# Performance work log

Hardware: AMD Instinct MI355X
Metric: run time of the kernel (lower is better)

## Reference

```python
import jax, jax.numpy as jnp
import numpy as np

B, S, D, H, F = 16, 512, 1024, 16, 4096
DH = D // H
LN_EPS = 1e-12


def layer_norm(x, g, b):
    mu = jnp.mean(x, axis=-1, keepdims=True)
    var = jnp.mean(jnp.square(x - mu), axis=-1, keepdims=True)
    return (x - mu) * jax.lax.rsqrt(var + LN_EPS) * g + b


def setup_inputs() -> dict:
    key = jax.random.key(0)
    ks = jax.random.split(key, 16)
    s_attn = 1.0 / np.sqrt(D)
    s_ffn = 1.0 / np.sqrt(F)
    return {
        "hidden_states": jax.random.normal(ks[0], (B, S, D), jnp.float32),
        "attention_mask": jnp.zeros((B, S), jnp.float32),
        # weights stored [in, out]
        "Wq": jax.random.normal(ks[1], (D, D), jnp.float32) * s_attn,
        "bq": jnp.zeros((D,), jnp.float32),
        "Wk": jax.random.normal(ks[2], (D, D), jnp.float32) * s_attn,
        "bk": jnp.zeros((D,), jnp.float32),
        "Wv": jax.random.normal(ks[3], (D, D), jnp.float32) * s_attn,
        "bv": jnp.zeros((D,), jnp.float32),
        "Wo": jax.random.normal(ks[4], (D, D), jnp.float32) * s_attn,
        "bo": jnp.zeros((D,), jnp.float32),
        "ln1_g": jnp.ones((D,), jnp.float32),
        "ln1_b": jnp.zeros((D,), jnp.float32),
        "Wi": jax.random.normal(ks[5], (D, F), jnp.float32) * s_attn,
        "bi": jnp.zeros((F,), jnp.float32),
        "Wo2": jax.random.normal(ks[6], (F, D), jnp.float32) * s_ffn,
        "bo2": jnp.zeros((D,), jnp.float32),
        "ln2_g": jnp.ones((D,), jnp.float32),
        "ln2_b": jnp.zeros((D,), jnp.float32),
    }


def reference(hidden_states, attention_mask, Wq, bq, Wk, bk, Wv, bv, Wo, bo,
              ln1_g, ln1_b, Wi, bi, Wo2, bo2, ln2_g, ln2_b):
    x = hidden_states
    # --- self attention ---
    q = (x @ Wq + bq).reshape(B, S, H, DH)
    k = (x @ Wk + bk).reshape(B, S, H, DH)
    v = (x @ Wv + bv).reshape(B, S, H, DH)
    scores = jnp.einsum("bqhd,bkhd->bhqk", q, k) / np.sqrt(DH)
    scores = scores + attention_mask[:, None, None, :]
    probs = jax.nn.softmax(scores, axis=-1)  # dropout p=0 (eval)
    ctx = jnp.einsum("bhqk,bkhd->bqhd", probs, v).reshape(B, S, D)
    # --- self output: dense + residual + LN ---
    attn_out = layer_norm(ctx @ Wo + bo + x, ln1_g, ln1_b)
    # --- intermediate: dense + gelu (exact erf gelu, BERT) ---
    inter = jax.nn.gelu(attn_out @ Wi + bi, approximate=False)
    # --- output: dense + residual + LN ---
    out = layer_norm(inter @ Wo2 + bo2 + attn_out, ln2_g, ln2_b)
    return out
```

## Files before the change

kernel.cpp:

```cpp
#include <hip/hip_runtime.h>
#include <hip/hip_bf16.h>
#include <math.h>

#define DEV_INLINE __device__ __forceinline__

typedef __attribute__((ext_vector_type(8))) short bf16x8;
typedef __attribute__((ext_vector_type(8))) unsigned short u16x8;
typedef __attribute__((ext_vector_type(4))) float f32x4;


DEV_INLINE void gload_lds16(const void* g, void* l) {
  __builtin_amdgcn_global_load_lds(
      (__attribute__((address_space(1))) unsigned int*)const_cast<void*>(g),
      (__attribute__((address_space(3))) unsigned int*)l,
      16, 0, 0);
}

DEV_INLINE short f2bs(float x) {
  union { __hip_bfloat16 h; short s; } u;
  u.h = __float2bfloat16(x);
  return u.s;
}

DEV_INLINE f32x4 mfma16(bf16x8 a, bf16x8 b, f32x4 c) {
  return __builtin_amdgcn_mfma_f32_16x16x32_bf16(a, b, c, 0, 0, 0);
}


__global__ __launch_bounds__(256)
void cvt_x_bf16(const float* __restrict__ in, __hip_bfloat16* __restrict__ out) {
  const size_t i = ((size_t)blockIdx.x * 256 + threadIdx.x) * 4;
  const float4 x = *(const float4*)(in + i);
  union { __hip_bfloat16 h[4]; ushort4 u; } pk;
  pk.h[0] = __float2bfloat16(x.x);
  pk.h[1] = __float2bfloat16(x.y);
  pk.h[2] = __float2bfloat16(x.z);
  pk.h[3] = __float2bfloat16(x.w);
  *(ushort4*)(out + i) = pk.u;
}

__global__ __launch_bounds__(256)
void transpose_w(const float* __restrict__ W, __hip_bfloat16* __restrict__ Wt, int K, int N) {
  __shared__ float t[32][33];
  const int n0 = blockIdx.x * 32, k0 = blockIdx.y * 32;
  const int tx = threadIdx.x & 31, ty = threadIdx.x >> 5;
#pragma unroll
  for (int r = ty; r < 32; r += 8)
    t[r][tx] = W[(size_t)(k0 + r) * N + n0 + tx];
  __syncthreads();
#pragma unroll
  for (int r = ty; r < 32; r += 8)
    Wt[(size_t)(n0 + r) * K + k0 + tx] = __float2bfloat16(t[tx][r]);
}

__global__ __launch_bounds__(256)
void concat_bias(const float* __restrict__ a, const float* __restrict__ b,
                 const float* __restrict__ c, float* __restrict__ o) {
  const int i = blockIdx.x * 256 + threadIdx.x;
  o[i] = a[i]; o[1024 + i] = b[i]; o[2048 + i] = c[i];
}


template<int MODE>
DEV_INLINE void gemm64_body(const short* __restrict__ A, const short* __restrict__ Bt,
                            const float* __restrict__ bias, const float* __restrict__ resid,
                            __hip_bfloat16* __restrict__ Cb, float* __restrict__ Cf,
                            int M, int N, int K)
{
  __shared__ __align__(128) short lds[16384];

  const int tid = threadIdx.x;
  const int lane = tid & 63, w = tid >> 6;
  const int q4 = lane >> 4, c16 = lane & 15;
  const int wm = (w >> 1) * 64, wn = (w & 1) * 64;

  const int nNT = N >> 7;
  int bid = blockIdx.x;
  { const int cpx = (int)gridDim.x >> 3; bid = (bid & 7) * cpx + (bid >> 3); }
  const int bm = (bid / nNT) * 128;
  const int bn = (bid % nNT) * 128;

  const int sr = tid >> 3, sl = tid & 7;
  const int sg = (sl ^ (sr & 7)) * 8;
  const short* pA = A  + (size_t)(bm + sr) * K + sg;
  const short* pB = Bt + (size_t)(bn + sr) * K + sg;
  char* const dA = (char*)lds + w * 1024;
  char* const dB = (char*)lds + 32768 / 2 * 2 / 2 + w * 1024;

  f32x4 acc[4][4];
#pragma unroll
  for (int i = 0; i < 4; ++i)
#pragma unroll
    for (int j = 0; j < 4; ++j) acc[i][j] = (f32x4){0.f, 0.f, 0.f, 0.f};

  char* const baseA = (char*)lds;
  char* const baseB = (char*)lds + 16384;

  for (int kt = 0; kt < K; kt += 64) {
    __syncthreads();
#pragma unroll
    for (int u = 0; u < 4; ++u) {
      gload_lds16(pA + (size_t)u * 32 * K + kt, baseA + u * 4096 + w * 1024);
      gload_lds16(pB + (size_t)u * 32 * K + kt, baseB + u * 4096 + w * 1024);
    }
    __syncthreads();

#pragma unroll
    for (int kk = 0; kk < 2; ++kk) {
      bf16x8 af[4], bfr[4];
#pragma unroll
      for (int mt = 0; mt < 4; ++mt)
        af[mt] = *(const bf16x8*)(baseA + (wm + mt * 16 + c16) * 128 +
                                  (((kk * 4 + q4) ^ (c16 & 7)) * 16));
#pragma unroll
      for (int nt = 0; nt < 4; ++nt)
        bfr[nt] = *(const bf16x8*)(baseB + (wn + nt * 16 + c16) * 128 +
                                   (((kk * 4 + q4) ^ (c16 & 7)) * 16));
#pragma unroll
      for (int mt = 0; mt < 4; ++mt)
#pragma unroll
        for (int nt = 0; nt < 4; ++nt)
          acc[mt][nt] = mfma16(af[mt], bfr[nt], acc[mt][nt]);
    }
  }

  __syncthreads();

  float* eb = (float*)((char*)lds + w * 4352);
  const int erow = lane >> 2, ecol = (lane & 3) * 16;
#pragma unroll
  for (int mf = 0; mf < 4; ++mf) {
#pragma unroll
    for (int nf = 0; nf < 4; ++nf) {
      const int col = bn + wn + nf * 16 + c16;
      const float bsv = bias[col];
#pragma unroll
      for (int j = 0; j < 4; ++j) {
        float v = acc[mf][nf][j] + bsv;
        if constexpr (MODE == 2)
          v = 0.5f * v * (1.0f + erff(v * 0.70710678118654752f));
        eb[(q4 * 4 + j) * 68 + nf * 16 + c16] = v;
      }
    }
    const int gr = bm + wm + mf * 16 + erow;
    const size_t gbase = (size_t)gr * N + bn + wn + ecol;
    if constexpr (MODE == 1) {
#pragma unroll
      for (int u = 0; u < 4; ++u) {
        float4 t = *(float4*)&eb[erow * 68 + ecol + u * 4];
        const float4 r = *(const float4*)&resid[gbase + u * 4];
        t.x += r.x; t.y += r.y; t.z += r.z; t.w += r.w;
        *(float4*)&Cf[gbase + u * 4] = t;
      }
    } else {
      unsigned short* cp = (unsigned short*)Cb;
#pragma unroll
      for (int u = 0; u < 2; ++u) {
        float4 a = *(float4*)&eb[erow * 68 + ecol + u * 8];
        float4 b = *(float4*)&eb[erow * 68 + ecol + u * 8 + 4];
        u16x8 o;
        o[0] = (unsigned short)f2bs(a.x); o[1] = (unsigned short)f2bs(a.y);
        o[2] = (unsigned short)f2bs(a.z); o[3] = (unsigned short)f2bs(a.w);
        o[4] = (unsigned short)f2bs(b.x); o[5] = (unsigned short)f2bs(b.y);
        o[6] = (unsigned short)f2bs(b.z); o[7] = (unsigned short)f2bs(b.w);
        *(u16x8*)(cp + gbase + u * 8) = o;
      }
    }
  }
}

__global__ __launch_bounds__(256)
void gemm_qkv(const short* A, const short* Bt, const float* bias,
              __hip_bfloat16* Cb, int M, int N, int K) {
  gemm64_body<0>(A, Bt, bias, nullptr, Cb, nullptr, M, N, K);
}
__global__ __launch_bounds__(256)
void gemm_wo(const short* A, const short* Bt, const float* bias,
             const float* resid, float* Cf, int M, int N, int K) {
  gemm64_body<1>(A, Bt, bias, resid, nullptr, Cf, M, N, K);
}
__global__ __launch_bounds__(256)
void gemm_wi(const short* A, const short* Bt, const float* bias,
             __hip_bfloat16* Cb, int M, int N, int K) {
  gemm64_body<2>(A, Bt, bias, nullptr, Cb, nullptr, M, N, K);
}
__global__ __launch_bounds__(256)
void gemm_wo2(const short* A, const short* Bt, const float* bias,
              const float* resid, float* Cf, int M, int N, int K) {
  gemm64_body<1>(A, Bt, bias, resid, nullptr, Cf, M, N, K);
}


__global__ __launch_bounds__(256)
void attn_flash(const short* __restrict__ Q, const short* __restrict__ Kmat,
                const short* __restrict__ V, const float* __restrict__ mask,
                __hip_bfloat16* __restrict__ ctx, int qs)
{
  __shared__ short Ksm[64 * 64];
  __shared__ short Vsm[64 * 64];
  __shared__ short Psm[4 * 16 * 64];

  const int tid = threadIdx.x;
  const int lane = tid & 63;
  const int w = tid >> 6;
  const int q4 = lane >> 4;
  const int c16 = lane & 15;
  const int b = blockIdx.z;
  const int h = blockIdx.y;
  const int qb = blockIdx.x;

  const size_t rowbase = (size_t)b * 512;
  const int hoff = h * 64;

  bf16x8 aq[2];
  {
    const size_t qrow = rowbase + (size_t)qb * 64 + w * 16 + c16;
    const short* qp = Q + qrow * qs + hoff + q4 * 8;
    aq[0] = *(const bf16x8*)(qp);
    aq[1] = *(const bf16x8*)(qp + 32);
  }

  float m_r[4], l_r[4];
  f32x4 O[4];
#pragma unroll
  for (int j = 0; j < 4; ++j) { m_r[j] = -INFINITY; l_r[j] = 0.f; O[j] = (f32x4){0.f, 0.f, 0.f, 0.f}; }

  const int kc0 = w * 128 + lane;
  const int kp0 = kc0 >> 3, kd0 = (kc0 & 7) * 8;
  const int kc1 = kc0 + 64;
  const int kp1 = kc1 >> 3, kd1 = (kc1 & 7) * 8;

  for (int kv0 = 0; kv0 < 512; kv0 += 64) {
    __syncthreads();
    gload_lds16(Kmat + (rowbase + kv0 + kp0) * qs + hoff + (kd0 ^ ((kp0 & 7) << 3)),
                (char*)Ksm + (size_t)(w * 128 + 0) * 16);
    gload_lds16(Kmat + (rowbase + kv0 + kp1) * qs + hoff + (kd1 ^ ((kp1 & 7) << 3)),
                (char*)Ksm + (size_t)(w * 128 + 64) * 16);
#pragma unroll
    for (int it = 0; it < 2; ++it) {
      const int c = tid + 256 * it;
      const int kp = c >> 3;
      const int dh8 = (c & 7) * 8;
      const bf16x8 vv = *(const bf16x8*)(V + (rowbase + kv0 + kp) * qs + hoff + dh8);
#pragma unroll
      for (int j = 0; j < 8; ++j) {
        const int dh = dh8 + j;
        *(short*)((char*)Vsm + dh * 128 + ((kp * 2) ^ ((dh & 7) << 4))) = vv[j];
      }
    }
    __syncthreads();

    float pv[4][4];
    float mk[4];
#pragma unroll
    for (int t = 0; t < 4; ++t) mk[t] = mask[rowbase + kv0 + t * 16 + c16];
#pragma unroll
    for (int t = 0; t < 4; ++t) {
      f32x4 z = (f32x4){0.f, 0.f, 0.f, 0.f};
      const int kp = t * 16 + c16;
#pragma unroll
      for (int ks = 0; ks < 2; ++ks) {
        const int d = ks * 32 + q4 * 8;
        bf16x8 kf = *(const bf16x8*)((char*)Ksm + kp * 128 + ((d * 2) ^ ((kp & 7) << 4)));
        z = mfma16(aq[ks], kf, z);
      }
#pragma unroll
      for (int j = 0; j < 4; ++j) pv[t][j] = z[j] * 0.125f + mk[t];
    }

#pragma unroll
    for (int j = 0; j < 4; ++j) {
      float mt_ = fmaxf(fmaxf(pv[0][j], pv[1][j]), fmaxf(pv[2][j], pv[3][j]));
#pragma unroll
      for (int o = 8; o >= 1; o >>= 1) mt_ = fmaxf(mt_, __shfl_xor(mt_, o));
      const float mn = fmaxf(m_r[j], mt_);
      const float sc = __expf(m_r[j] - mn);
      float rs = 0.f;
#pragma unroll
      for (int t = 0; t < 4; ++t) { const float pe = __expf(pv[t][j] - mn); pv[t][j] = pe; rs += pe; }
#pragma unroll
      for (int o = 8; o >= 1; o >>= 1) rs += __shfl_xor(rs, o);
      l_r[j] = l_r[j] * sc + rs;
      m_r[j] = mn;
#pragma unroll
      for (int nt = 0; nt < 4; ++nt) O[nt][j] *= sc;
    }

    char* pb = (char*)Psm + w * 2048;
#pragma unroll
    for (int j = 0; j < 4; ++j) {
      const int r = q4 * 4 + j;
#pragma unroll
      for (int t = 0; t < 4; ++t) {
        const int ck = t * 16 + c16;
        *(short*)(pb + r * 128 + ((ck * 2) ^ ((r & 7) << 4))) = f2bs(pv[t][j]);
      }
    }

#pragma unroll
    for (int ks = 0; ks < 2; ++ks) {
      const int kk = ks * 32 + q4 * 8;
      bf16x8 pa = *(const bf16x8*)(pb + c16 * 128 + ((kk * 2) ^ ((c16 & 7) << 4)));
#pragma unroll
      for (int nt = 0; nt < 4; ++nt) {
        const int dh = nt * 16 + c16;
        bf16x8 vf = *(const bf16x8*)((char*)Vsm + dh * 128 + ((kk * 2) ^ ((dh & 7) << 4)));
        O[nt] = mfma16(pa, vf, O[nt]);
      }
    }
  }

  float rinv[4];
#pragma unroll
  for (int j = 0; j < 4; ++j) rinv[j] = 1.0f / l_r[j];
#pragma unroll
  for (int nt = 0; nt < 4; ++nt) {
#pragma unroll
    for (int j = 0; j < 4; ++j) {
      const size_t row = rowbase + (size_t)qb * 64 + w * 16 + q4 * 4 + j;
      ctx[row * 1024 + hoff + nt * 16 + c16] = __float2bfloat16(O[nt][j] * rinv[j]);
    }
  }
}


DEV_INLINE void ln_body(const float* __restrict__ in, const float* __restrict__ gam,
                        const float* __restrict__ bet, float* __restrict__ outf,
                        __hip_bfloat16* __restrict__ outb)
{
  const int row = blockIdx.x;
  const int tid = threadIdx.x;
  const size_t base = (size_t)row * 1024 + tid * 4;
  const float4 x = *(const float4*)(in + base);
  float s  = x.x + x.y + x.z + x.w;
  float s2 = x.x * x.x + x.y * x.y + x.z * x.z + x.w * x.w;
#pragma unroll
  for (int o = 32; o >= 1; o >>= 1) { s += __shfl_xor(s, o); s2 += __shfl_xor(s2, o); }
  __shared__ float sb[8];
  const int w = tid >> 6;
  if ((tid & 63) == 0) { sb[w] = s; sb[w + 4] = s2; }
  __syncthreads();
  const float ts  = sb[0] + sb[1] + sb[2] + sb[3];
  const float ts2 = sb[4] + sb[5] + sb[6] + sb[7];
  const float mu = ts * (1.0f / 1024.0f);
  const float var = ts2 * (1.0f / 1024.0f) - mu * mu;
  const float rstd = rsqrtf(var + 1e-12f);
  const float4 g4 = *(const float4*)(gam + tid * 4);
  const float4 b4 = *(const float4*)(bet + tid * 4);
  const float y0 = (x.x - mu) * rstd * g4.x + b4.x;
  const float y1 = (x.y - mu) * rstd * g4.y + b4.y;
  const float y2 = (x.z - mu) * rstd * g4.z + b4.z;
  const float y3 = (x.w - mu) * rstd * g4.w + b4.w;
  if (outf) {
    float4 y; y.x = y0; y.y = y1; y.z = y2; y.w = y3;
    *(float4*)(outf + base) = y;
  }
  if (outb) {
    union { __hip_bfloat16 h[4]; ushort4 u; } pk;
    pk.h[0] = __float2bfloat16(y0);
    pk.h[1] = __float2bfloat16(y1);
    pk.h[2] = __float2bfloat16(y2);
    pk.h[3] = __float2bfloat16(y3);
    *(ushort4*)(outb + base) = pk.u;
  }
}

__global__ __launch_bounds__(256)
void ln_attn(const float* in, const float* gam, const float* bet,
             float* outf, __hip_bfloat16* outb) { ln_body(in, gam, bet, outf, outb); }
__global__ __launch_bounds__(256)
void ln_ffn(const float* in, const float* gam, const float* bet, float* outf) {
  ln_body(in, gam, bet, outf, nullptr);
}


extern "C" void kernel_launch(void* const* d_in, const int* in_sizes, int n_in,
                              void* d_out, int out_size, void* d_ws, size_t ws_size,
                              hipStream_t stream)
{
  const float* X    = (const float*)d_in[0];
  const float* mask = (const float*)d_in[1];
  const float* Wq   = (const float*)d_in[2];   const float* bq  = (const float*)d_in[3];
  const float* Wk   = (const float*)d_in[4];   const float* bk  = (const float*)d_in[5];
  const float* Wv   = (const float*)d_in[6];   const float* bv  = (const float*)d_in[7];
  const float* Wo   = (const float*)d_in[8];   const float* bo  = (const float*)d_in[9];
  const float* g1   = (const float*)d_in[10];  const float* b1  = (const float*)d_in[11];
  const float* Wi   = (const float*)d_in[12];  const float* bi  = (const float*)d_in[13];
  const float* Wo2  = (const float*)d_in[14];  const float* bo2 = (const float*)d_in[15];
  const float* g2   = (const float*)d_in[16];  const float* b2  = (const float*)d_in[17];
  float* out = (float*)d_out;
  (void)in_sizes; (void)n_in; (void)out_size; (void)ws_size;

  const size_t D = 1024, F = 4096;
  const size_t MN = 8192 * D;

  char* p = (char*)d_ws;
  auto alloc = [&](size_t bytes) { char* r = p; p += (bytes + 255) & ~(size_t)255; return r; };
  short* Xb    = (short*)alloc(MN * 2);
  short* QKVb  = (short*)alloc(8192 * 3072 * 2);
  short* WqkvT = (short*)alloc(3072 * D * 2);
  short* WoT   = (short*)alloc(D * D * 2);
  short* WiT   = (short*)alloc(D * F * 2);
  short* Wo2T  = (short*)alloc(D * F * 2);
  float* bqkv  = (float*)alloc(3072 * 4);
  float* A1f   = (float*)alloc(MN * 4);
  short* I1    = (short*)alloc(8192 * F * 2);

  cvt_x_bf16<<<dim3((unsigned)(MN / 1024)), 256, 0, stream>>>(X, (__hip_bfloat16*)Xb);
  transpose_w<<<dim3(32, 32),  256, 0, stream>>>(Wq,  (__hip_bfloat16*)(WqkvT + 0),           1024, 1024);
  transpose_w<<<dim3(32, 32),  256, 0, stream>>>(Wk,  (__hip_bfloat16*)(WqkvT + 1024 * 1024), 1024, 1024);
  transpose_w<<<dim3(32, 32),  256, 0, stream>>>(Wv,  (__hip_bfloat16*)(WqkvT + 2048 * 1024), 1024, 1024);
  transpose_w<<<dim3(32, 32),  256, 0, stream>>>(Wo,  (__hip_bfloat16*)WoT,  1024, 1024);
  transpose_w<<<dim3(128, 32), 256, 0, stream>>>(Wi,  (__hip_bfloat16*)WiT,  1024, 4096);
  transpose_w<<<dim3(32, 128), 256, 0, stream>>>(Wo2, (__hip_bfloat16*)Wo2T, 4096, 1024);
  concat_bias<<<dim3(4), 256, 0, stream>>>(bq, bk, bv, bqkv);

  gemm_qkv<<<dim3(1536), 256, 0, stream>>>(Xb, WqkvT, bqkv, (__hip_bfloat16*)QKVb, 8192, 3072, 1024);

  attn_flash<<<dim3(8, 16, 16), 256, 0, stream>>>(QKVb, QKVb + 1024, QKVb + 2048, mask,
                                                  (__hip_bfloat16*)Xb, 3072);

  gemm_wo<<<dim3(512), 256, 0, stream>>>(Xb, WoT, bo, X, out, 8192, 1024, 1024);
  ln_attn<<<dim3(8192), 256, 0, stream>>>(out, g1, b1, A1f, (__hip_bfloat16*)QKVb);

  gemm_wi<<<dim3(2048), 256, 0, stream>>>(QKVb, WiT, bi, (__hip_bfloat16*)I1, 8192, 4096, 1024);

  gemm_wo2<<<dim3(512), 256, 0, stream>>>(I1, Wo2T, bo2, A1f, out, 8192, 1024, 4096);
  ln_ffn<<<dim3(8192), 256, 0, stream>>>(out, g2, b2, out);
}
```

Before: 441.1 us.

## Double-buffer GEMM LDS tiles and issue hand-scheduled ds_read plus MFMA blocks

Doubles the GEMM shared-memory buffer so the next K-tile's global-to-LDS loads are issued before computing on the current tile, with one barrier per iteration instead of two. Fragment reads become inline-asm ds_read_b128 with immediate offsets from precomputed swizzled base addresses, which flip between buffers by XOR. The MFMA block is wrapped in sched barriers and raised wave priority. The goal is to hide global load latency behind matrix math. The cost is twice the LDS per block, which may lower occupancy, plus fragile manual scheduling through inline asm.

```diff
diff --git a/kernel.cpp b/kernel.cpp
--- a/kernel.cpp
+++ b/kernel.cpp
@@ -16,6 +16,10 @@
       16, 0, 0);
 }
 
+DEV_INLINE unsigned lds_a(const void* p) {
+  return (unsigned)(unsigned long long)(__attribute__((address_space(3))) const void*)p;
+}
+
 DEV_INLINE short f2bs(float x) {
   union { __hip_bfloat16 h; short s; } u;
   u.h = __float2bfloat16(x);
@@ -25,6 +29,9 @@
 DEV_INLINE f32x4 mfma16(bf16x8 a, bf16x8 b, f32x4 c) {
   return __builtin_amdgcn_mfma_f32_16x16x32_bf16(a, b, c, 0, 0, 0);
 }
+
+#define DSREAD_O(dst, base, imm) \
+  asm volatile("ds_read_b128 %0, %1 offset:%2" : "=v"(dst) : "v"(base), "n"(imm))
 
 
 __global__ __launch_bounds__(256)
@@ -67,7 +74,7 @@
                             __hip_bfloat16* __restrict__ Cb, float* __restrict__ Cf,
                             int M, int N, int K)
 {
-  __shared__ __align__(128) short lds[16384];
+  __shared__ __align__(128) short lds[32768];
 
   const int tid = threadIdx.x;
   const int lane = tid & 63, w = tid >> 6;
@@ -84,8 +91,13 @@
   const int sg = (sl ^ (sr & 7)) * 8;
   const short* pA = A  + (size_t)(bm + sr) * K + sg;
   const short* pB = Bt + (size_t)(bn + sr) * K + sg;
-  char* const dA = (char*)lds + w * 1024;
-  char* const dB = (char*)lds + 32768 / 2 * 2 / 2 + w * 1024;
+
+  const int s0 = (q4 ^ (c16 & 7)) * 16;
+  const int s1 = ((q4 ^ 4) ^ (c16 & 7)) * 16;
+  unsigned aRd0 = lds_a(lds) + (unsigned)((wm + c16) * 128 + s0);
+  unsigned aRd1 = lds_a(lds) + (unsigned)((wm + c16) * 128 + s1);
+  unsigned bRd0 = lds_a(lds) + (unsigned)(16384 + (wn + c16) * 128 + s0);
+  unsigned bRd1 = lds_a(lds) + (unsigned)(16384 + (wn + c16) * 128 + s1);
 
   f32x4 acc[4][4];
 #pragma unroll
@@ -93,38 +105,60 @@
 #pragma unroll
     for (int j = 0; j < 4; ++j) acc[i][j] = (f32x4){0.f, 0.f, 0.f, 0.f};
 
-  char* const baseA = (char*)lds;
-  char* const baseB = (char*)lds + 16384;
-
-  for (int kt = 0; kt < K; kt += 64) {
+  auto stage = [&](int buf, int kt) {
+    char* b = (char*)lds + buf * 32768;
+#pragma unroll
+    for (int u = 0; u < 4; ++u) {
+      gload_lds16(pA + (size_t)u * 32 * K + kt, b + u * 4096 + w * 1024);
+      gload_lds16(pB + (size_t)u * 32 * K + kt, b + 16384 + u * 4096 + w * 1024);
+    }
+  };
+
+  stage(0, 0);
+  __syncthreads();
+
+  const int NT = K >> 6;
+  int cur = 0;
+  for (int t = 0; t < NT; ++t) {
+    __builtin_amdgcn_sched_barrier(0);
+    if (t + 1 < NT) stage(cur ^ 1, (t + 1) << 6);
+    __builtin_amdgcn_sched_barrier(0);
+
+    bf16x8 a0, a1, a2, a3, a4, a5, a6, a7;
+    bf16x8 b0, b1, b2, b3, b4, b5, b6, b7;
+    DSREAD_O(a0, aRd0, 0 * 2048); DSREAD_O(a1, aRd0, 1 * 2048);
+    DSREAD_O(a2, aRd0, 2 * 2048); DSREAD_O(a3, aRd0, 3 * 2048);
+    DSREAD_O(b0, bRd0, 0 * 2048); DSREAD_O(b1, bRd0, 1 * 2048);
+    DSREAD_O(b2, bRd0, 2 * 2048); DSREAD_O(b3, bRd0, 3 * 2048);
+    DSREAD_O(a4, aRd1, 0 * 2048); DSREAD_O(a5, aRd1, 1 * 2048);
+    DSREAD_O(a6, aRd1, 2 * 2048); DSREAD_O(a7, aRd1, 3 * 2048);
+    DSREAD_O(b4, bRd1, 0 * 2048); DSREAD_O(b5, bRd1, 1 * 2048);
+    DSREAD_O(b6, bRd1, 2 * 2048); DSREAD_O(b7, bRd1, 3 * 2048);
+
+    asm volatile("s_waitcnt lgkmcnt(0)");
+    __builtin_amdgcn_sched_barrier(0);
+    __builtin_amdgcn_s_setprio(1);
+    acc[0][0] = mfma16(a0, b0, acc[0][0]); acc[0][1] = mfma16(a0, b1, acc[0][1]);
+    acc[0][2] = mfma16(a0, b2, acc[0][2]); acc[0][3] = mfma16(a0, b3, acc[0][3]);
+    acc[1][0] = mfma16(a1, b0, acc[1][0]); acc[1][1] = mfma16(a1, b1, acc[1][1]);
+    acc[1][2] = mfma16(a1, b2, acc[1][2]); acc[1][3] = mfma16(a1, b3, acc[1][3]);
+    acc[2][0] = mfma16(a2, b0, acc[2][0]); acc[2][1] = mfma16(a2, b1, acc[2][1]);
+    acc[2][2] = mfma16(a2, b2, acc[2][2]); acc[2][3] = mfma16(a2, b3, acc[2][3]);
+    acc[3][0] = mfma16(a3, b0, acc[3][0]); acc[3][1] = mfma16(a3, b1, acc[3][1]);
+    acc[3][2] = mfma16(a3, b2, acc[3][2]); acc[3][3] = mfma16(a3, b3, acc[3][3]);
+    acc[0][0] = mfma16(a4, b4, acc[0][0]); acc[0][1] = mfma16(a4, b5, acc[0][1]);
+    acc[0][2] = mfma16(a4, b6, acc[0][2]); acc[0][3] = mfma16(a4, b7, acc[0][3]);
+    acc[1][0] = mfma16(a5, b4, acc[1][0]); acc[1][1] = mfma16(a5, b5, acc[1][1]);
+    acc[1][2] = mfma16(a5, b6, acc[1][2]); acc[1][3] = mfma16(a5, b7, acc[1][3]);
+    acc[2][0] = mfma16(a6, b4, acc[2][0]); acc[2][1] = mfma16(a6, b5, acc[2][1]);
+    acc[2][2] = mfma16(a6, b6, acc[2][2]); acc[2][3] = mfma16(a6, b7, acc[2][3]);
+    acc[3][0] = mfma16(a7, b4, acc[3][0]); acc[3][1] = mfma16(a7, b5, acc[3][1]);
+    acc[3][2] = mfma16(a7, b6, acc[3][2]); acc[3][3] = mfma16(a7, b7, acc[3][3]);
+    __builtin_amdgcn_s_setprio(0);
+
     __syncthreads();
-#pragma unroll
-    for (int u = 0; u < 4; ++u) {
-      gload_lds16(pA + (size_t)u * 32 * K + kt, baseA + u * 4096 + w * 1024);
-      gload_lds16(pB + (size_t)u * 32 * K + kt, baseB + u * 4096 + w * 1024);
-    }
-    __syncthreads();
-
-#pragma unroll
-    for (int kk = 0; kk < 2; ++kk) {
-      bf16x8 af[4], bfr[4];
-#pragma unroll
-      for (int mt = 0; mt < 4; ++mt)
-        af[mt] = *(const bf16x8*)(baseA + (wm + mt * 16 + c16) * 128 +
-                                  (((kk * 4 + q4) ^ (c16 & 7)) * 16));
-#pragma unroll
-      for (int nt = 0; nt < 4; ++nt)
-        bfr[nt] = *(const bf16x8*)(baseB + (wn + nt * 16 + c16) * 128 +
-                                   (((kk * 4 + q4) ^ (c16 & 7)) * 16));
-#pragma unroll
-      for (int mt = 0; mt < 4; ++mt)
-#pragma unroll
-        for (int nt = 0; nt < 4; ++nt)
-          acc[mt][nt] = mfma16(af[mt], bfr[nt], acc[mt][nt]);
-    }
-  }
-
-  __syncthreads();
+    aRd0 ^= 0x8000; aRd1 ^= 0x8000; bRd0 ^= 0x8000; bRd1 ^= 0x8000; cur ^= 1;
+  }
 
   float* eb = (float*)((char*)lds + w * 4352);
   const int erow = lane >> 2, ecol = (lane & 3) * 16;
```

After: 422.8 us. -4.1%, faster.
